# Kernel optimization log

Measured on AMD Instinct MI355X. Metric: run time of the kernel, lower is better.

The kernel has to match this reference:

```python
import jax, jax.numpy as jnp
import numpy as np

B, T, IN, H = 64, 256, 512, 1024


def setup_inputs() -> dict:
    key = jax.random.key(0)
    ks = jax.random.split(key, 21)
    stdv = 1.0 / float(np.sqrt(H))
    u = lambda k, shape: jax.random.uniform(k, shape, jnp.float32, -stdv, stdv)
    inp = {"input": jax.random.normal(ks[0], (B, T, IN), jnp.float32)}
    idx = 1
    for g in ("f", "i", "o", "c"):
        inp[f"W_{g}"] = u(ks[idx], (H, IN)); idx += 1
        inp[f"W_{g}_mask"] = u(ks[idx], (H, IN)); idx += 1
        inp[f"U_{g}"] = u(ks[idx], (H, H)); idx += 1
        inp[f"U_{g}_mask"] = u(ks[idx], (H, H)); idx += 1
        inp[f"b_{g}"] = u(ks[idx], (H,)); idx += 1
    return inp


def reference(input, W_f, W_f_mask, U_f, U_f_mask, b_f,
              W_i, W_i_mask, U_i, U_i_mask, b_i,
              W_o, W_o_mask, U_o, U_o_mask, b_o,
              W_c, W_c_mask, U_c, U_c_mask, b_c):
    # MaskedParameterMatrix with wise='feat': sigmoid(x @ W_mask^T) * (x @ W^T)
    def ml(x, W, Wm):
        return jax.nn.sigmoid(x @ Wm.T) * (x @ W.T)

    def step(carry, x_t):  # x_t: [B, IN]
        h, c = carry  # each [B, H]
        f = jax.nn.sigmoid(ml(x_t, W_f, W_f_mask) + ml(h, U_f, U_f_mask) + b_f)
        # NOTE: original module computes the input gate but never uses it (bug kept for fidelity)
        i = jax.nn.sigmoid(ml(x_t, W_i, W_i_mask) + ml(h, U_i, U_i_mask) + b_i)
        o = jax.nn.sigmoid(ml(x_t, W_o, W_o_mask) + ml(h, U_o, U_o_mask) + b_o)
        c = f * c + jnp.tanh(ml(x_t, W_c, W_c_mask) + ml(h, U_c, U_c_mask) + b_c)
        h = o * c
        return (h, c), h

    b, hdim = input.shape[0], W_f.shape[0]
    h0 = jnp.zeros((b, hdim), input.dtype)
    (hT, cT), ys = jax.lax.scan(step, (h0, h0), jnp.swapaxes(input, 0, 1))
    output = jnp.swapaxes(ys, 0, 1)  # [B, T, H]
    # final states shaped [1, B, H] as in the torch module (after transpose)
    return output, (hT[None], cT[None])
```

## Files before the change

kernel.cpp:

```cpp
#include <hip/hip_runtime.h>
#include <hip/hip_bf16.h>


typedef __attribute__((ext_vector_type(8))) short bfrag;
typedef __attribute__((ext_vector_type(4))) float f32x4;

__device__ __forceinline__ unsigned short f2b(float v) {
  __hip_bfloat16 h = __float2bfloat16(v);
  union { __hip_bfloat16 h; unsigned short u; } c; c.h = h; return c.u;
}
__device__ __forceinline__ float b2f(unsigned short u) {
  union { unsigned int i; float f; } c; c.i = ((unsigned int)u) << 16; return c.f;
}
__device__ __forceinline__ float sigm(float x) { return 1.0f / (1.0f + __expf(-x)); }
__device__ __forceinline__ float tanh_f(float x) {
  float e = __expf(2.0f * x);
  return (e - 1.0f) / (e + 1.0f);
}

__global__ __launch_bounds__(512, 2) void xproj_kernel(
    const float* __restrict__ inp,
    const float* __restrict__ Wf, const float* __restrict__ Wmf,
    const float* __restrict__ Wo, const float* __restrict__ Wmo,
    const float* __restrict__ Wc, const float* __restrict__ Wmc,
    unsigned short* __restrict__ mlx)
{
  __shared__ unsigned short Al[256 * 128];
  __shared__ unsigned short Bl[256 * 128];

  const int tid = threadIdx.x;
  const int w = tid >> 6, l = tid & 63;
  const int c = l & 15, g4 = l >> 4;
  const int jc = blockIdx.x, gate = blockIdx.y, tq = blockIdx.z;
  const float* W  = (gate == 0) ? Wf  : (gate == 1) ? Wo  : Wc;
  const float* Wm = (gate == 0) ? Wmf : (gate == 1) ? Wmo : Wmc;
  const int j0 = jc * 128;

  f32x4 acc[2][16];
#pragma unroll
  for (int mi = 0; mi < 2; ++mi)
#pragma unroll
    for (int ni = 0; ni < 16; ++ni) acc[mi][ni] = (f32x4){0.f, 0.f, 0.f, 0.f};

  for (int kc = 0; kc < 4; ++kc) {
#pragma unroll
    for (int i = 0; i < 16; ++i) {
      int idx = tid + i * 512;
      int row = idx >> 5;
      int xl  = idx & 31;
      int b_ = row & 63, tl = row >> 6;
      const float4 va = *(const float4*)(inp + (size_t)(b_ * 256 + tq * 4 + tl) * 512 + kc * 128 + xl * 4);
      ushort4 pa;
      pa.x = f2b(va.x); pa.y = f2b(va.y); pa.z = f2b(va.z); pa.w = f2b(va.w);
      *(ushort4*)((char*)Al + ((row * 256 + xl * 8) ^ ((row & 7) << 4))) = pa;
      const float* src = (row < 128) ? (W + (size_t)(j0 + row) * 512)
                                     : (Wm + (size_t)(j0 + row - 128) * 512);
      const float4 vb = *(const float4*)(src + kc * 128 + xl * 4);
      ushort4 pb;
      pb.x = f2b(vb.x); pb.y = f2b(vb.y); pb.z = f2b(vb.z); pb.w = f2b(vb.w);
      *(ushort4*)((char*)Bl + ((row * 256 + xl * 8) ^ ((row & 7) << 4))) = pb;
    }
    __syncthreads();
#pragma unroll
    for (int ks = 0; ks < 4; ++ks) {
      const int koff = (ks * 32 + g4 * 8) * 2;
      bfrag af[2];
#pragma unroll
      for (int mi = 0; mi < 2; ++mi) {
        int row = w * 32 + mi * 16 + c;
        af[mi] = *(const bfrag*)((const char*)Al + ((row * 256 + koff) ^ ((row & 7) << 4)));
      }
#pragma unroll
      for (int ni = 0; ni < 16; ++ni) {
        int n = ni * 16 + c;
        bfrag bf = *(const bfrag*)((const char*)Bl + ((n * 256 + koff) ^ ((n & 7) << 4)));
#pragma unroll
        for (int mi = 0; mi < 2; ++mi)
          acc[mi][ni] = __builtin_amdgcn_mfma_f32_16x16x32_bf16(af[mi], bf, acc[mi][ni], 0, 0, 0);
      }
    }
    __syncthreads();
  }
#pragma unroll
  for (int mi = 0; mi < 2; ++mi) {
#pragma unroll
    for (int ni = 0; ni < 8; ++ni) {
      f32x4 xw = acc[mi][ni];
      f32x4 xm = acc[mi][ni + 8];
      ushort4 st;
      st.x = f2b(xw[0] * sigm(xm[0]));
      st.y = f2b(xw[1] * sigm(xm[1]));
      st.z = f2b(xw[2] * sigm(xm[2]));
      st.w = f2b(xw[3] * sigm(xm[3]));
      int row = w * 32 + mi * 16 + g4 * 4;
      int tl = row >> 6, b_ = row & 63;
      int j = j0 + ni * 16 + c;
      size_t addr = ((size_t)((tq * 4 + tl) * 3 + gate) * 1024 + j) * 64 + b_;
      *(ushort4*)(mlx + addr) = st;
    }
  }
}

__global__ __launch_bounds__(256, 1) void recur_kernel(
    const float* __restrict__ Uf, const float* __restrict__ Umf,
    const float* __restrict__ Uo, const float* __restrict__ Umo,
    const float* __restrict__ Uc, const float* __restrict__ Umc,
    const float* __restrict__ bfp, const float* __restrict__ bop,
    const float* __restrict__ bcp,
    const unsigned short* __restrict__ mlx,
    unsigned short* __restrict__ hx,
    float* __restrict__ cfin,
    unsigned int* __restrict__ sent)
{
  __shared__ float prep[2][4 * 48 * 68];

  __builtin_amdgcn_fence(__ATOMIC_ACQUIRE, "agent");

  const int tid = threadIdx.x;
  const int bid = blockIdx.x;
  const int w = tid >> 6, l = tid & 63;
  const int c = l & 15, g4 = l >> 4;
  const int j0 = bid * 8;

  bfrag Breg[3][8];
#pragma unroll
  for (int nt = 0; nt < 3; ++nt) {
    const int n = nt * 16 + c;
    const int mi6 = n >> 3;
    const float* src = (mi6 == 0) ? Uf : (mi6 == 1) ? Umf : (mi6 == 2) ? Uo
                     : (mi6 == 3) ? Umo : (mi6 == 4) ? Uc : Umc;
    src += (size_t)(j0 + (n & 7)) * 1024;
#pragma unroll
    for (int ks = 0; ks < 8; ++ks) {
      const int k = w * 256 + ks * 32 + g4 * 8;
      const float4 v0 = *(const float4*)(src + k);
      const float4 v1 = *(const float4*)(src + k + 4);
      bfrag b;
      b[0] = (short)f2b(v0.x); b[1] = (short)f2b(v0.y);
      b[2] = (short)f2b(v0.z); b[3] = (short)f2b(v0.w);
      b[4] = (short)f2b(v1.x); b[5] = (short)f2b(v1.y);
      b[6] = (short)f2b(v1.z); b[7] = (short)f2b(v1.w);
      Breg[nt][ks] = b;
    }
  }

  const int bb = l;
  const int cl0 = w * 2;
  float bias[2][3], cr[2] = {0.f, 0.f};
  float mf[2], mo[2], mc[2];
#pragma unroll
  for (int q = 0; q < 2; ++q) {
    bias[q][0] = bfp[j0 + cl0 + q];
    bias[q][1] = bop[j0 + cl0 + q];
    bias[q][2] = bcp[j0 + cl0 + q];
  }
  {
    size_t mb = (size_t)(j0 + cl0) * 64 + bb;
#pragma unroll
    for (int q = 0; q < 2; ++q) {
      mf[q] = b2f(mlx[mb + q * 64]);
      mo[q] = b2f(mlx[mb + 65536 + q * 64]);
      mc[q] = b2f(mlx[mb + 2 * 65536 + q * 64]);
    }
  }

  for (int t = 0; t < 256; ++t) {
    if (t > 0) {
      const unsigned long long* sp =
          (const unsigned long long*)(sent + (size_t)t * 512 + w * 128 + 2 * l);
      while (true) {
        unsigned long long v = __hip_atomic_load(sp, __ATOMIC_RELAXED, __HIP_MEMORY_SCOPE_AGENT);
        if (__all(v == 0x0000000100000001ULL)) break;
      }
      __builtin_amdgcn_sched_barrier(0);
      asm volatile("" ::: "memory");
    }

    f32x4 acc[4][3];
#pragma unroll
    for (int mi = 0; mi < 4; ++mi)
#pragma unroll
      for (int nt = 0; nt < 3; ++nt) acc[mi][nt] = (f32x4){0.f, 0.f, 0.f, 0.f};

#pragma unroll
    for (int ks = 0; ks < 8; ++ks) {
      const int kb = w * 32 + ks * 4 + g4;
#pragma unroll
      for (int mi = 0; mi < 4; ++mi) {
        const bfrag af = *(const bfrag*)(hx + (((size_t)t * 128 + kb) * 64 + mi * 16 + c) * 8);
#pragma unroll
        for (int nt = 0; nt < 3; ++nt)
          acc[mi][nt] = __builtin_amdgcn_mfma_f32_16x16x32_bf16(af, Breg[nt][ks], acc[mi][nt], 0, 0, 0);
      }
    }
    float* pp = prep[t & 1];
#pragma unroll
    for (int mi = 0; mi < 4; ++mi)
#pragma unroll
      for (int nt = 0; nt < 3; ++nt) {
        int col = nt * 16 + c;
        *(f32x4*)&pp[(w * 48 + col) * 68 + mi * 16 + g4 * 4] = acc[mi][nt];
      }
    __syncthreads();

    unsigned int pack = 0;
#pragma unroll
    for (int q = 0; q < 2; ++q) {
      const int cl = cl0 + q;
      float s[6];
#pragma unroll
      for (int m = 0; m < 6; ++m) {
        const int col = m * 8 + cl;
        s[m] = pp[col * 68 + bb] + pp[(48 + col) * 68 + bb] +
               pp[(96 + col) * 68 + bb] + pp[(144 + col) * 68 + bb];
      }
      float fg = sigm(mf[q] + sigm(s[1]) * s[0] + bias[q][0]);
      float og = sigm(mo[q] + sigm(s[3]) * s[2] + bias[q][1]);
      float cd = tanh_f(mc[q] + sigm(s[5]) * s[4] + bias[q][2]);
      cr[q] = fg * cr[q] + cd;
      float hv = og * cr[q];
      pack |= (unsigned int)f2b(hv) << (16 * q);
      if (t == 255) cfin[(size_t)(j0 + cl) * 64 + bb] = cr[q];
    }
    __hip_atomic_store(
        (unsigned int*)(hx + ((((size_t)(t + 1) * 128 + bid) * 64 + bb) * 8 + cl0)),
        pack, __ATOMIC_RELAXED, __HIP_MEMORY_SCOPE_AGENT);

    asm volatile("s_waitcnt vmcnt(0)" ::: "memory");
    if (l == 0)
      __hip_atomic_store(&sent[(size_t)(t + 1) * 512 + bid * 4 + w], 1u,
                         __ATOMIC_RELAXED, __HIP_MEMORY_SCOPE_AGENT);

    if (t < 255) {
      size_t mb = (size_t)(t + 1) * 3 * 65536 + (size_t)(j0 + cl0) * 64 + bb;
#pragma unroll
      for (int q = 0; q < 2; ++q) {
        mf[q] = b2f(mlx[mb + q * 64]);
        mo[q] = b2f(mlx[mb + 65536 + q * 64]);
        mc[q] = b2f(mlx[mb + 2 * 65536 + q * 64]);
      }
    }
  }
}

__global__ __launch_bounds__(128) void histcast_kernel(
    const unsigned short* __restrict__ hx, float* __restrict__ out)
{
  const int b = blockIdx.x >> 8, t = blockIdx.x & 255;
  const int j = threadIdx.x * 8;
  const unsigned short* src = hx + (((size_t)(t + 1) * 128 + (j >> 3)) * 64 + b) * 8;
  float* dst = out + ((size_t)b * 256 + t) * 1024 + j;
  ushort4 v0 = *(const ushort4*)(src);
  ushort4 v1 = *(const ushort4*)(src + 4);
  float4 o0, o1;
  o0.x = b2f(v0.x); o0.y = b2f(v0.y); o0.z = b2f(v0.z); o0.w = b2f(v0.w);
  o1.x = b2f(v1.x); o1.y = b2f(v1.y); o1.z = b2f(v1.z); o1.w = b2f(v1.w);
  *(float4*)(dst) = o0;
  *(float4*)(dst + 4) = o1;
}

__global__ __launch_bounds__(256) void finals_kernel(
    const unsigned short* __restrict__ hx, const float* __restrict__ cfin,
    float* __restrict__ out)
{
  int tid = blockIdx.x * 256 + threadIdx.x;
  int b = tid >> 10, j = tid & 1023;
  out[16777216 + tid]         = b2f(hx[(((size_t)256 * 128 + (j >> 3)) * 64 + b) * 8 + (j & 7)]);
  out[16777216 + 65536 + tid] = cfin[(size_t)j * 64 + b];
}

extern "C" void kernel_launch(void* const* d_in, const int* in_sizes, int n_in,
                              void* d_out, int out_size, void* d_ws, size_t ws_size,
                              hipStream_t stream)
{
  const float* input = (const float*)d_in[0];
  const float* W_f  = (const float*)d_in[1];
  const float* Wm_f = (const float*)d_in[2];
  const float* U_f  = (const float*)d_in[3];
  const float* Um_f = (const float*)d_in[4];
  const float* b_f  = (const float*)d_in[5];
  const float* W_o  = (const float*)d_in[11];
  const float* Wm_o = (const float*)d_in[12];
  const float* U_o  = (const float*)d_in[13];
  const float* Um_o = (const float*)d_in[14];
  const float* b_o  = (const float*)d_in[15];
  const float* W_c  = (const float*)d_in[16];
  const float* Wm_c = (const float*)d_in[17];
  const float* U_c  = (const float*)d_in[18];
  const float* Um_c = (const float*)d_in[19];
  const float* b_c  = (const float*)d_in[20];

  char* ws = (char*)d_ws;
  size_t off = 0;
  unsigned short* mlx = (unsigned short*)(ws + off); off += (size_t)256 * 3 * 1024 * 64 * 2;
  unsigned short* hx  = (unsigned short*)(ws + off); off += (size_t)257 * 128 * 64 * 8 * 2;
  float* cfin = (float*)(ws + off);                  off += (size_t)1024 * 64 * 4;
  unsigned int* sent = (unsigned int*)(ws + off);    off += (size_t)257 * 512 * 4;
  if (off > ws_size) return;

  hipMemsetAsync(hx, 0, 131072, stream);
  hipMemsetAsync(sent, 0, (size_t)257 * 512 * 4, stream);

  xproj_kernel<<<dim3(8, 3, 64), 512, 0, stream>>>(input, W_f, Wm_f, W_o, Wm_o, W_c, Wm_c, mlx);
  recur_kernel<<<128, 256, 0, stream>>>(U_f, Um_f, U_o, Um_o, U_c, Um_c,
                                        b_f, b_o, b_c, mlx, hx, cfin, sent);
  histcast_kernel<<<16384, 128, 0, stream>>>(hx, (float*)d_out);
  finals_kernel<<<256, 256, 0, stream>>>(hx, cfin, (float*)d_out);
}
```

Baseline: 2.271 ms.

## Replace sentinel-flag handshake with data-as-flag polling on hidden state

Removes the separate per-step sentinel array. The hidden-state buffer is now pre-filled with 0xFF and consumers spin directly on the h values until no 32-bit word is all-ones, so the data itself acts as the ready signal. This drops the vmcnt wait and flag store on the producer side and one round trip of latency per step. The mask-projection loads are moved to the top of each step. The cost is a large extra memset of the history buffer and a correctness assumption that two adjacent bf16 values never both encode 0xFFFF (a NaN pattern).

```diff
diff --git a/kernel.cpp b/kernel.cpp
--- a/kernel.cpp
+++ b/kernel.cpp
@@ -109,8 +109,7 @@
     const float* __restrict__ bcp,
     const unsigned short* __restrict__ mlx,
     unsigned short* __restrict__ hx,
-    float* __restrict__ cfin,
-    unsigned int* __restrict__ sent)
+    float* __restrict__ cfin)
 {
   __shared__ float prep[2][4 * 48 * 68];
 
@@ -147,33 +146,23 @@
   const int bb = l;
   const int cl0 = w * 2;
   float bias[2][3], cr[2] = {0.f, 0.f};
-  float mf[2], mo[2], mc[2];
 #pragma unroll
   for (int q = 0; q < 2; ++q) {
     bias[q][0] = bfp[j0 + cl0 + q];
     bias[q][1] = bop[j0 + cl0 + q];
     bias[q][2] = bcp[j0 + cl0 + q];
   }
-  {
-    size_t mb = (size_t)(j0 + cl0) * 64 + bb;
-#pragma unroll
-    for (int q = 0; q < 2; ++q) {
-      mf[q] = b2f(mlx[mb + q * 64]);
-      mo[q] = b2f(mlx[mb + 65536 + q * 64]);
-      mc[q] = b2f(mlx[mb + 2 * 65536 + q * 64]);
-    }
-  }
 
   for (int t = 0; t < 256; ++t) {
-    if (t > 0) {
-      const unsigned long long* sp =
-          (const unsigned long long*)(sent + (size_t)t * 512 + w * 128 + 2 * l);
-      while (true) {
-        unsigned long long v = __hip_atomic_load(sp, __ATOMIC_RELAXED, __HIP_MEMORY_SCOPE_AGENT);
-        if (__all(v == 0x0000000100000001ULL)) break;
-      }
-      __builtin_amdgcn_sched_barrier(0);
-      asm volatile("" ::: "memory");
+    float mfv[2], mov[2], mcv[2];
+    {
+      size_t mb = (size_t)t * 3 * 65536 + (size_t)(j0 + cl0) * 64 + bb;
+#pragma unroll
+      for (int q = 0; q < 2; ++q) {
+        mfv[q] = b2f(mlx[mb + q * 64]);
+        mov[q] = b2f(mlx[mb + 65536 + q * 64]);
+        mcv[q] = b2f(mlx[mb + 2 * 65536 + q * 64]);
+      }
     }
 
     f32x4 acc[4][3];
@@ -185,14 +174,35 @@
 #pragma unroll
     for (int ks = 0; ks < 8; ++ks) {
       const int kb = w * 32 + ks * 4 + g4;
+      const unsigned long long* rowp =
+          (const unsigned long long*)(hx + (((size_t)t * 128 + kb) * 64 + c) * 8);
+      unsigned long long q0[4], q1[4];
+      while (true) {
+        bool ok = true;
+#pragma unroll
+        for (int mi = 0; mi < 4; ++mi) {
+          q0[mi] = __hip_atomic_load(rowp + mi * 32,     __ATOMIC_RELAXED, __HIP_MEMORY_SCOPE_AGENT);
+          q1[mi] = __hip_atomic_load(rowp + mi * 32 + 1, __ATOMIC_RELAXED, __HIP_MEMORY_SCOPE_AGENT);
+        }
+#pragma unroll
+        for (int mi = 0; mi < 4; ++mi) {
+          ok = ok && ((unsigned)(q0[mi])       != 0xFFFFFFFFu)
+                  && ((unsigned)(q0[mi] >> 32) != 0xFFFFFFFFu)
+                  && ((unsigned)(q1[mi])       != 0xFFFFFFFFu)
+                  && ((unsigned)(q1[mi] >> 32) != 0xFFFFFFFFu);
+        }
+        if (__all(ok)) break;
+      }
 #pragma unroll
       for (int mi = 0; mi < 4; ++mi) {
-        const bfrag af = *(const bfrag*)(hx + (((size_t)t * 128 + kb) * 64 + mi * 16 + c) * 8);
+        union { unsigned long long q[2]; bfrag f; } u;
+        u.q[0] = q0[mi]; u.q[1] = q1[mi];
 #pragma unroll
         for (int nt = 0; nt < 3; ++nt)
-          acc[mi][nt] = __builtin_amdgcn_mfma_f32_16x16x32_bf16(af, Breg[nt][ks], acc[mi][nt], 0, 0, 0);
-      }
-    }
+          acc[mi][nt] = __builtin_amdgcn_mfma_f32_16x16x32_bf16(u.f, Breg[nt][ks], acc[mi][nt], 0, 0, 0);
+      }
+    }
+
     float* pp = prep[t & 1];
 #pragma unroll
     for (int mi = 0; mi < 4; ++mi)
@@ -214,9 +224,9 @@
         s[m] = pp[col * 68 + bb] + pp[(48 + col) * 68 + bb] +
                pp[(96 + col) * 68 + bb] + pp[(144 + col) * 68 + bb];
       }
-      float fg = sigm(mf[q] + sigm(s[1]) * s[0] + bias[q][0]);
-      float og = sigm(mo[q] + sigm(s[3]) * s[2] + bias[q][1]);
-      float cd = tanh_f(mc[q] + sigm(s[5]) * s[4] + bias[q][2]);
+      float fg = sigm(mfv[q] + sigm(s[1]) * s[0] + bias[q][0]);
+      float og = sigm(mov[q] + sigm(s[3]) * s[2] + bias[q][1]);
+      float cd = tanh_f(mcv[q] + sigm(s[5]) * s[4] + bias[q][2]);
       cr[q] = fg * cr[q] + cd;
       float hv = og * cr[q];
       pack |= (unsigned int)f2b(hv) << (16 * q);
@@ -225,21 +235,6 @@
     __hip_atomic_store(
         (unsigned int*)(hx + ((((size_t)(t + 1) * 128 + bid) * 64 + bb) * 8 + cl0)),
         pack, __ATOMIC_RELAXED, __HIP_MEMORY_SCOPE_AGENT);
-
-    asm volatile("s_waitcnt vmcnt(0)" ::: "memory");
-    if (l == 0)
-      __hip_atomic_store(&sent[(size_t)(t + 1) * 512 + bid * 4 + w], 1u,
-                         __ATOMIC_RELAXED, __HIP_MEMORY_SCOPE_AGENT);
-
-    if (t < 255) {
-      size_t mb = (size_t)(t + 1) * 3 * 65536 + (size_t)(j0 + cl0) * 64 + bb;
-#pragma unroll
-      for (int q = 0; q < 2; ++q) {
-        mf[q] = b2f(mlx[mb + q * 64]);
-        mo[q] = b2f(mlx[mb + 65536 + q * 64]);
-        mc[q] = b2f(mlx[mb + 2 * 65536 + q * 64]);
-      }
-    }
   }
 }
 
@@ -295,15 +290,14 @@
   unsigned short* mlx = (unsigned short*)(ws + off); off += (size_t)256 * 3 * 1024 * 64 * 2;
   unsigned short* hx  = (unsigned short*)(ws + off); off += (size_t)257 * 128 * 64 * 8 * 2;
   float* cfin = (float*)(ws + off);                  off += (size_t)1024 * 64 * 4;
-  unsigned int* sent = (unsigned int*)(ws + off);    off += (size_t)257 * 512 * 4;
   if (off > ws_size) return;
 
   hipMemsetAsync(hx, 0, 131072, stream);
-  hipMemsetAsync(sent, 0, (size_t)257 * 512 * 4, stream);
+  hipMemsetAsync((char*)hx + 131072, 0xFF, (size_t)256 * 131072, stream);
 
   xproj_kernel<<<dim3(8, 3, 64), 512, 0, stream>>>(input, W_f, Wm_f, W_o, Wm_o, W_c, Wm_c, mlx);
   recur_kernel<<<128, 256, 0, stream>>>(U_f, Um_f, U_o, Um_o, U_c, Um_c,
-                                        b_f, b_o, b_c, mlx, hx, cfin, sent);
+                                        b_f, b_o, b_c, mlx, hx, cfin);
   histcast_kernel<<<16384, 128, 0, stream>>>(hx, (float*)d_out);
   finals_kernel<<<256, 256, 0, stream>>>(hx, cfin, (float*)d_out);
 }
```

After: 2.405 ms. 5.9% more time.

## Move recurrent weights to swizzled LDS, batch h loads, coalesce h stores via LDS

Applied to the files above, without the earlier changes.

Recurrent weight fragments now live in an XOR-swizzled LDS buffer instead of registers, and are read per k-step during the MFMA loop. All h fragments for a step are loaded up front before any MFMA. Each wave's packed h outputs are gathered in LDS and written as 64-bit atomic stores by 16 lanes instead of 32-bit stores from every lane. The double-buffered prep array becomes single-buffered, and the per-step mlx loads move before the spin-wait. The aim is to free registers and raise memory-level parallelism, at the cost of extra LDS traffic and an added __syncthreads per step on the serial critical path.

```diff
diff --git a/kernel.cpp b/kernel.cpp
--- a/kernel.cpp
+++ b/kernel.cpp
@@ -112,7 +112,9 @@
     float* __restrict__ cfin,
     unsigned int* __restrict__ sent)
 {
-  __shared__ float prep[2][4 * 48 * 68];
+  __shared__ unsigned short Blds[48 * 1024];
+  __shared__ float prep[4 * 48 * 68];
+  __shared__ unsigned int hshare[64 * 4];
 
   __builtin_amdgcn_fence(__ATOMIC_ACQUIRE, "agent");
 
@@ -122,49 +124,49 @@
   const int c = l & 15, g4 = l >> 4;
   const int j0 = bid * 8;
 
-  bfrag Breg[3][8];
-#pragma unroll
-  for (int nt = 0; nt < 3; ++nt) {
-    const int n = nt * 16 + c;
-    const int mi6 = n >> 3;
-    const float* src = (mi6 == 0) ? Uf : (mi6 == 1) ? Umf : (mi6 == 2) ? Uo
-                     : (mi6 == 3) ? Umo : (mi6 == 4) ? Uc : Umc;
-    src += (size_t)(j0 + (n & 7)) * 1024;
-#pragma unroll
-    for (int ks = 0; ks < 8; ++ks) {
-      const int k = w * 256 + ks * 32 + g4 * 8;
-      const float4 v0 = *(const float4*)(src + k);
-      const float4 v1 = *(const float4*)(src + k + 4);
-      bfrag b;
-      b[0] = (short)f2b(v0.x); b[1] = (short)f2b(v0.y);
-      b[2] = (short)f2b(v0.z); b[3] = (short)f2b(v0.w);
-      b[4] = (short)f2b(v1.x); b[5] = (short)f2b(v1.y);
-      b[6] = (short)f2b(v1.z); b[7] = (short)f2b(v1.w);
-      Breg[nt][ks] = b;
+  {
+    const float* mats[6] = {Uf, Umf, Uo, Umo, Uc, Umc};
+    const int rbase = tid >> 4;
+    const int sub = tid & 15;
+#pragma unroll
+    for (int rep = 0; rep < 3; ++rep) {
+      int r = rep * 16 + rbase;
+      const float* src = mats[r >> 3] + (size_t)(j0 + (r & 7)) * 1024;
+#pragma unroll
+      for (int i = 0; i < 16; ++i) {
+        int k = sub * 64 + i * 4;
+        float4 v = *(const float4*)(src + k);
+        ushort4 p;
+        p.x = f2b(v.x); p.y = f2b(v.y); p.z = f2b(v.z); p.w = f2b(v.w);
+        *(ushort4*)((char*)Blds + (((r * 1024 + k) * 2) ^ ((r & 7) << 4))) = p;
+      }
     }
   }
 
   const int bb = l;
   const int cl0 = w * 2;
   float bias[2][3], cr[2] = {0.f, 0.f};
-  float mf[2], mo[2], mc[2];
 #pragma unroll
   for (int q = 0; q < 2; ++q) {
     bias[q][0] = bfp[j0 + cl0 + q];
     bias[q][1] = bop[j0 + cl0 + q];
     bias[q][2] = bcp[j0 + cl0 + q];
   }
-  {
-    size_t mb = (size_t)(j0 + cl0) * 64 + bb;
-#pragma unroll
-    for (int q = 0; q < 2; ++q) {
-      mf[q] = b2f(mlx[mb + q * 64]);
-      mo[q] = b2f(mlx[mb + 65536 + q * 64]);
-      mc[q] = b2f(mlx[mb + 2 * 65536 + q * 64]);
-    }
-  }
+  const int kb0 = (w * 256 + g4 * 8) * 2;
+  __syncthreads();
 
   for (int t = 0; t < 256; ++t) {
+    float mfv[2], mov[2], mcv[2];
+    {
+      size_t mb = (size_t)t * 3 * 65536 + (size_t)(j0 + cl0) * 64 + bb;
+#pragma unroll
+      for (int q = 0; q < 2; ++q) {
+        mfv[q] = b2f(mlx[mb + q * 64]);
+        mov[q] = b2f(mlx[mb + 65536 + q * 64]);
+        mcv[q] = b2f(mlx[mb + 2 * 65536 + q * 64]);
+      }
+    }
+
     if (t > 0) {
       const unsigned long long* sp =
           (const unsigned long long*)(sent + (size_t)t * 512 + w * 128 + 2 * l);
@@ -176,30 +178,44 @@
       asm volatile("" ::: "memory");
     }
 
-    f32x4 acc[4][3];
-#pragma unroll
-    for (int mi = 0; mi < 4; ++mi)
-#pragma unroll
-      for (int nt = 0; nt < 3; ++nt) acc[mi][nt] = (f32x4){0.f, 0.f, 0.f, 0.f};
-
+    bfrag af[8][4];
 #pragma unroll
     for (int ks = 0; ks < 8; ++ks) {
       const int kb = w * 32 + ks * 4 + g4;
-#pragma unroll
-      for (int mi = 0; mi < 4; ++mi) {
-        const bfrag af = *(const bfrag*)(hx + (((size_t)t * 128 + kb) * 64 + mi * 16 + c) * 8);
+      const unsigned short* rp = hx + (((size_t)t * 128 + kb) * 64 + c) * 8;
+#pragma unroll
+      for (int mi = 0; mi < 4; ++mi)
+        af[ks][mi] = *(const bfrag*)(rp + mi * 16 * 8);
+    }
+
+    f32x4 acc[4][3];
+#pragma unroll
+    for (int mi = 0; mi < 4; ++mi)
+#pragma unroll
+      for (int nt = 0; nt < 3; ++nt) acc[mi][nt] = (f32x4){0.f, 0.f, 0.f, 0.f};
+
+#pragma unroll
+    for (int ks = 0; ks < 8; ++ks) {
+      const int kb2 = kb0 + ks * 64;
+      bfrag bfr[3];
+#pragma unroll
+      for (int nt = 0; nt < 3; ++nt) {
+        const int n = nt * 16 + c;
+        bfr[nt] = *(const bfrag*)((const char*)Blds + (n * 2048 + (kb2 ^ ((n & 7) << 4))));
+      }
+#pragma unroll
+      for (int mi = 0; mi < 4; ++mi)
 #pragma unroll
         for (int nt = 0; nt < 3; ++nt)
-          acc[mi][nt] = __builtin_amdgcn_mfma_f32_16x16x32_bf16(af, Breg[nt][ks], acc[mi][nt], 0, 0, 0);
-      }
-    }
-    float* pp = prep[t & 1];
+          acc[mi][nt] = __builtin_amdgcn_mfma_f32_16x16x32_bf16(af[ks][mi], bfr[nt], acc[mi][nt], 0, 0, 0);
+    }
+
 #pragma unroll
     for (int mi = 0; mi < 4; ++mi)
 #pragma unroll
       for (int nt = 0; nt < 3; ++nt) {
         int col = nt * 16 + c;
-        *(f32x4*)&pp[(w * 48 + col) * 68 + mi * 16 + g4 * 4] = acc[mi][nt];
+        *(f32x4*)&prep[(w * 48 + col) * 68 + mi * 16 + g4 * 4] = acc[mi][nt];
       }
     __syncthreads();
 
@@ -211,35 +227,35 @@
 #pragma unroll
       for (int m = 0; m < 6; ++m) {
         const int col = m * 8 + cl;
-        s[m] = pp[col * 68 + bb] + pp[(48 + col) * 68 + bb] +
-               pp[(96 + col) * 68 + bb] + pp[(144 + col) * 68 + bb];
-      }
-      float fg = sigm(mf[q] + sigm(s[1]) * s[0] + bias[q][0]);
-      float og = sigm(mo[q] + sigm(s[3]) * s[2] + bias[q][1]);
-      float cd = tanh_f(mc[q] + sigm(s[5]) * s[4] + bias[q][2]);
+        s[m] = prep[col * 68 + bb] + prep[(48 + col) * 68 + bb] +
+               prep[(96 + col) * 68 + bb] + prep[(144 + col) * 68 + bb];
+      }
+      float fg = sigm(mfv[q] + sigm(s[1]) * s[0] + bias[q][0]);
+      float og = sigm(mov[q] + sigm(s[3]) * s[2] + bias[q][1]);
+      float cd = tanh_f(mcv[q] + sigm(s[5]) * s[4] + bias[q][2]);
       cr[q] = fg * cr[q] + cd;
       float hv = og * cr[q];
       pack |= (unsigned int)f2b(hv) << (16 * q);
       if (t == 255) cfin[(size_t)(j0 + cl) * 64 + bb] = cr[q];
     }
-    __hip_atomic_store(
-        (unsigned int*)(hx + ((((size_t)(t + 1) * 128 + bid) * 64 + bb) * 8 + cl0)),
-        pack, __ATOMIC_RELAXED, __HIP_MEMORY_SCOPE_AGENT);
-
+
+    hshare[bb * 4 + w] = pack;
+    __syncthreads();
+
+    if (l < 16) {
+      const int row = w * 16 + l;
+      const uint4 hv4 = *(const uint4*)&hshare[row * 4];
+      unsigned long long q0 = ((unsigned long long)hv4.y << 32) | hv4.x;
+      unsigned long long q1 = ((unsigned long long)hv4.w << 32) | hv4.z;
+      unsigned long long* dst =
+          (unsigned long long*)(hx + ((((size_t)(t + 1) * 128 + bid) * 64 + row) * 8));
+      __hip_atomic_store(dst,     q0, __ATOMIC_RELAXED, __HIP_MEMORY_SCOPE_AGENT);
+      __hip_atomic_store(dst + 1, q1, __ATOMIC_RELAXED, __HIP_MEMORY_SCOPE_AGENT);
+    }
     asm volatile("s_waitcnt vmcnt(0)" ::: "memory");
     if (l == 0)
       __hip_atomic_store(&sent[(size_t)(t + 1) * 512 + bid * 4 + w], 1u,
                          __ATOMIC_RELAXED, __HIP_MEMORY_SCOPE_AGENT);
-
-    if (t < 255) {
-      size_t mb = (size_t)(t + 1) * 3 * 65536 + (size_t)(j0 + cl0) * 64 + bb;
-#pragma unroll
-      for (int q = 0; q < 2; ++q) {
-        mf[q] = b2f(mlx[mb + q * 64]);
-        mo[q] = b2f(mlx[mb + 65536 + q * 64]);
-        mc[q] = b2f(mlx[mb + 2 * 65536 + q * 64]);
-      }
-    }
   }
 }
 
```

Result: slower. 2.640 ms (+16.2%).

## Split batch into four 16-row groups and pipeline recurrence across them per wave

Applied to the files above, without the earlier changes.

The recurrent kernel now gives each wave two hidden columns over the full K dimension, with all 32 K-chunks of U held in registers. The batch is split into four independent 16-row groups that are processed in a staggered software pipeline. While one group's MFMA runs, the previous group's gate math, h store and flag signalling proceed, and the next group's flags are polled. This removes the cross-wave LDS reduction and the block-wide __syncthreads, and hides the inter-block flag latency behind independent work. In exchange it uses many more registers, finer-grained flags (four times as many sync points) and a changed hx layout.

```diff
diff --git a/kernel.cpp b/kernel.cpp
--- a/kernel.cpp
+++ b/kernel.cpp
@@ -112,7 +112,7 @@
     float* __restrict__ cfin,
     unsigned int* __restrict__ sent)
 {
-  __shared__ float prep[2][4 * 48 * 68];
+  __shared__ float ldsT[4][16][17];
 
   __builtin_amdgcn_fence(__ATOMIC_ACQUIRE, "agent");
 
@@ -120,127 +120,138 @@
   const int bid = blockIdx.x;
   const int w = tid >> 6, l = tid & 63;
   const int c = l & 15, g4 = l >> 4;
-  const int j0 = bid * 8;
-
-  bfrag Breg[3][8];
-#pragma unroll
-  for (int nt = 0; nt < 3; ++nt) {
-    const int n = nt * 16 + c;
-    const int mi6 = n >> 3;
-    const float* src = (mi6 == 0) ? Uf : (mi6 == 1) ? Umf : (mi6 == 2) ? Uo
-                     : (mi6 == 3) ? Umo : (mi6 == 4) ? Uc : Umc;
-    src += (size_t)(j0 + (n & 7)) * 1024;
-#pragma unroll
-    for (int ks = 0; ks < 8; ++ks) {
-      const int k = w * 256 + ks * 32 + g4 * 8;
-      const float4 v0 = *(const float4*)(src + k);
-      const float4 v1 = *(const float4*)(src + k + 4);
-      bfrag b;
-      b[0] = (short)f2b(v0.x); b[1] = (short)f2b(v0.y);
-      b[2] = (short)f2b(v0.z); b[3] = (short)f2b(v0.w);
-      b[4] = (short)f2b(v1.x); b[5] = (short)f2b(v1.y);
-      b[6] = (short)f2b(v1.z); b[7] = (short)f2b(v1.w);
-      Breg[nt][ks] = b;
+  const int W = bid * 4 + w;
+  const int r = c;
+  const int q = g4 & 1;
+
+  bfrag Breg[32];
+  {
+    const int m = c >> 1, q2 = c & 1;
+    const float* up = (m == 0) ? Uf : (m == 1) ? Umf : (m == 2) ? Uo
+                    : (m == 3) ? Umo : (m == 4) ? Uc : Umc;
+    const float* src = up + (size_t)(2 * W + q2) * 1024;
+    const bool pad = (c >= 12);
+#pragma unroll
+    for (int kc = 0; kc < 32; ++kc) {
+      bfrag b = {0, 0, 0, 0, 0, 0, 0, 0};
+      if (!pad) {
+        const float4 v0 = *(const float4*)(src + kc * 32 + g4 * 8);
+        const float4 v1 = *(const float4*)(src + kc * 32 + g4 * 8 + 4);
+        b[0] = (short)f2b(v0.x); b[1] = (short)f2b(v0.y);
+        b[2] = (short)f2b(v0.z); b[3] = (short)f2b(v0.w);
+        b[4] = (short)f2b(v1.x); b[5] = (short)f2b(v1.y);
+        b[6] = (short)f2b(v1.z); b[7] = (short)f2b(v1.w);
+      }
+      Breg[kc] = b;
     }
   }
-
-  const int bb = l;
-  const int cl0 = w * 2;
-  float bias[2][3], cr[2] = {0.f, 0.f};
-  float mf[2], mo[2], mc[2];
-#pragma unroll
-  for (int q = 0; q < 2; ++q) {
-    bias[q][0] = bfp[j0 + cl0 + q];
-    bias[q][1] = bop[j0 + cl0 + q];
-    bias[q][2] = bcp[j0 + cl0 + q];
+  const float bf_ = bfp[2 * W + q], bo_ = bop[2 * W + q], bc_ = bcp[2 * W + q];
+
+  bfrag af[32];
+  f32x4 accA = {0.f,0.f,0.f,0.f}, accB = {0.f,0.f,0.f,0.f};
+  float crA = 0.f, crB = 0.f, crC = 0.f, crD = 0.f;
+  unsigned long long P0[4] = {0,0,0,0}, P1[4] = {0,0,0,0};
+  float mA0=0.f,mA1=0.f,mA2=0.f, mB0=0.f,mB1=0.f,mB2=0.f;
+  const unsigned long long SOK = 0x0000000100000001ULL;
+
+#define SLOT(Pp, ACCP, ACCC, CR, MI0, MI1, MI2, MO0, MO1, MO2, PCHK, PNEW)     \
+  do {                                                                         \
+    const int s_ = t4 * 4 + (Pp);                                              \
+              \
+    if (t4 > 0) {                                                              \
+      f32x4 c0={0.f,0.f,0.f,0.f}, c1={0.f,0.f,0.f,0.f};                        \
+      f32x4 c2={0.f,0.f,0.f,0.f}, c3={0.f,0.f,0.f,0.f};                        \
+      _Pragma("unroll")                                                        \
+      for (int kc = 0; kc < 32; kc += 4) {                                     \
+        c0 = __builtin_amdgcn_mfma_f32_16x16x32_bf16(af[kc+0], Breg[kc+0], c0, 0,0,0); \
+        c1 = __builtin_amdgcn_mfma_f32_16x16x32_bf16(af[kc+1], Breg[kc+1], c1, 0,0,0); \
+        c2 = __builtin_amdgcn_mfma_f32_16x16x32_bf16(af[kc+2], Breg[kc+2], c2, 0,0,0); \
+        c3 = __builtin_amdgcn_mfma_f32_16x16x32_bf16(af[kc+3], Breg[kc+3], c3, 0,0,0); \
+      }                                                                        \
+      ACCC = (c0 + c1) + (c2 + c3);                                            \
+    } else {                                                                   \
+      ACCC = (f32x4){0.f, 0.f, 0.f, 0.f};                                      \
+    }                                                                          \
+         \
+    asm volatile("s_waitcnt vmcnt(0)" ::: "memory");                           \
+    if (s_ >= 2 && l == 0)                                                     \
+      __hip_atomic_store(&sent[(size_t)(s_ + 2) * 512 + W], 1u,                \
+                         __ATOMIC_RELAXED, __HIP_MEMORY_SCOPE_AGENT);          \
+         \
+    if ((s_ + 1) >= 4 && (s_ + 1) <= 1023) {                                   \
+      while (true) {                                                           \
+        bool ok = (PCHK[0] == SOK) && (PCHK[1] == SOK) &&                      \
+                  (PCHK[2] == SOK) && (PCHK[3] == SOK);                        \
+        if (__all(ok)) break;                                                  \
+        const unsigned long long* pp =                                         \
+            (const unsigned long long*)(sent + (size_t)(s_ + 1) * 512) + 4*l;  \
+        PCHK[0] = __hip_atomic_load(pp+0, __ATOMIC_RELAXED, __HIP_MEMORY_SCOPE_AGENT); \
+        PCHK[1] = __hip_atomic_load(pp+1, __ATOMIC_RELAXED, __HIP_MEMORY_SCOPE_AGENT); \
+        PCHK[2] = __hip_atomic_load(pp+2, __ATOMIC_RELAXED, __HIP_MEMORY_SCOPE_AGENT); \
+        PCHK[3] = __hip_atomic_load(pp+3, __ATOMIC_RELAXED, __HIP_MEMORY_SCOPE_AGENT); \
+      }                                                                        \
+      __builtin_amdgcn_sched_barrier(0);                                       \
+      asm volatile("" ::: "memory");                                           \
+      const unsigned short* ap = hx + (size_t)(s_ + 1) * 16384 + c * 1024 + g4 * 8; \
+      _Pragma("unroll")                                                        \
+      for (int kc = 0; kc < 32; ++kc) af[kc] = *(const bfrag*)(ap + kc * 32);  \
+    }                                                                          \
+            \
+    if (s_ >= 1) {                                                             \
+      const int tl = ((Pp) >= 1) ? t4 : (t4 - 1);                              \
+      const int gl = ((Pp) + 3) & 3;                                           \
+      ldsT[w][g4 * 4 + 0][c] = ACCP[0];                                        \
+      ldsT[w][g4 * 4 + 1][c] = ACCP[1];                                        \
+      ldsT[w][g4 * 4 + 2][c] = ACCP[2];                                        \
+      ldsT[w][g4 * 4 + 3][c] = ACCP[3];                                        \
+      float s0 = ldsT[w][r][0 + q], s1 = ldsT[w][r][2 + q];                    \
+      float s2 = ldsT[w][r][4 + q], s3 = ldsT[w][r][6 + q];                    \
+      float s4 = ldsT[w][r][8 + q], s5 = ldsT[w][r][10 + q];                   \
+      float fg = sigm((MI0) + sigm(s1) * s0 + bf_);                            \
+      float og = sigm((MI1) + sigm(s3) * s2 + bo_);                            \
+      float cd = tanh_f((MI2) + sigm(s5) * s4 + bc_);                          \
+      CR = fg * CR + cd;                                                       \
+      float hv = og * CR;                                                      \
+      unsigned int hvu = f2b(hv);                                              \
+      unsigned int hi = (unsigned int)__shfl((int)hvu, (l + 16) & 63, 64);     \
+      unsigned int pack = (hvu & 0xFFFFu) | (hi << 16);                        \
+      if (l < 16)                                                              \
+        __hip_atomic_store(                                                    \
+            (unsigned int*)(hx + (size_t)(s_ + 3) * 16384 + l * 1024 + 2 * W), \
+            pack, __ATOMIC_RELAXED, __HIP_MEMORY_SCOPE_AGENT);                 \
+      if (tl == 255 && l < 32)                                                 \
+        cfin[(size_t)(2 * W + q) * 64 + gl * 16 + r] = CR;                     \
+    }                                                                          \
+                                            \
+    if ((s_ + 2) >= 4 && (s_ + 2) <= 1023) {                                   \
+      const unsigned long long* pp =                                           \
+          (const unsigned long long*)(sent + (size_t)(s_ + 2) * 512) + 4 * l;  \
+      PNEW[0] = __hip_atomic_load(pp+0, __ATOMIC_RELAXED, __HIP_MEMORY_SCOPE_AGENT); \
+      PNEW[1] = __hip_atomic_load(pp+1, __ATOMIC_RELAXED, __HIP_MEMORY_SCOPE_AGENT); \
+      PNEW[2] = __hip_atomic_load(pp+2, __ATOMIC_RELAXED, __HIP_MEMORY_SCOPE_AGENT); \
+      PNEW[3] = __hip_atomic_load(pp+3, __ATOMIC_RELAXED, __HIP_MEMORY_SCOPE_AGENT); \
+    }                                                                          \
+                \
+    if (s_ <= 1023) {                                                          \
+      size_t mb = ((size_t)t4 * 3 * 1024 + (2 * W + q)) * 64 + (Pp) * 16 + r;  \
+      MO0 = b2f(mlx[mb]);                                                      \
+      MO1 = b2f(mlx[mb + 65536]);                                              \
+      MO2 = b2f(mlx[mb + 131072]);                                             \
+    }                                                                          \
+  } while (0)
+
+#pragma unroll 1
+  for (int t4 = 0; t4 < 256; ++t4) {
+    SLOT(0, accB, accA, crD, mB0, mB1, mB2, mA0, mA1, mA2, P1, P0);
+    SLOT(1, accA, accB, crA, mA0, mA1, mA2, mB0, mB1, mB2, P0, P1);
+    SLOT(2, accB, accA, crB, mB0, mB1, mB2, mA0, mA1, mA2, P1, P0);
+    SLOT(3, accA, accB, crC, mA0, mA1, mA2, mB0, mB1, mB2, P0, P1);
   }
   {
-    size_t mb = (size_t)(j0 + cl0) * 64 + bb;
-#pragma unroll
-    for (int q = 0; q < 2; ++q) {
-      mf[q] = b2f(mlx[mb + q * 64]);
-      mo[q] = b2f(mlx[mb + 65536 + q * 64]);
-      mc[q] = b2f(mlx[mb + 2 * 65536 + q * 64]);
-    }
-  }
-
-  for (int t = 0; t < 256; ++t) {
-    if (t > 0) {
-      const unsigned long long* sp =
-          (const unsigned long long*)(sent + (size_t)t * 512 + w * 128 + 2 * l);
-      while (true) {
-        unsigned long long v = __hip_atomic_load(sp, __ATOMIC_RELAXED, __HIP_MEMORY_SCOPE_AGENT);
-        if (__all(v == 0x0000000100000001ULL)) break;
-      }
-      __builtin_amdgcn_sched_barrier(0);
-      asm volatile("" ::: "memory");
-    }
-
-    f32x4 acc[4][3];
-#pragma unroll
-    for (int mi = 0; mi < 4; ++mi)
-#pragma unroll
-      for (int nt = 0; nt < 3; ++nt) acc[mi][nt] = (f32x4){0.f, 0.f, 0.f, 0.f};
-
-#pragma unroll
-    for (int ks = 0; ks < 8; ++ks) {
-      const int kb = w * 32 + ks * 4 + g4;
-#pragma unroll
-      for (int mi = 0; mi < 4; ++mi) {
-        const bfrag af = *(const bfrag*)(hx + (((size_t)t * 128 + kb) * 64 + mi * 16 + c) * 8);
-#pragma unroll
-        for (int nt = 0; nt < 3; ++nt)
-          acc[mi][nt] = __builtin_amdgcn_mfma_f32_16x16x32_bf16(af, Breg[nt][ks], acc[mi][nt], 0, 0, 0);
-      }
-    }
-    float* pp = prep[t & 1];
-#pragma unroll
-    for (int mi = 0; mi < 4; ++mi)
-#pragma unroll
-      for (int nt = 0; nt < 3; ++nt) {
-        int col = nt * 16 + c;
-        *(f32x4*)&pp[(w * 48 + col) * 68 + mi * 16 + g4 * 4] = acc[mi][nt];
-      }
-    __syncthreads();
-
-    unsigned int pack = 0;
-#pragma unroll
-    for (int q = 0; q < 2; ++q) {
-      const int cl = cl0 + q;
-      float s[6];
-#pragma unroll
-      for (int m = 0; m < 6; ++m) {
-        const int col = m * 8 + cl;
-        s[m] = pp[col * 68 + bb] + pp[(48 + col) * 68 + bb] +
-               pp[(96 + col) * 68 + bb] + pp[(144 + col) * 68 + bb];
-      }
-      float fg = sigm(mf[q] + sigm(s[1]) * s[0] + bias[q][0]);
-      float og = sigm(mo[q] + sigm(s[3]) * s[2] + bias[q][1]);
-      float cd = tanh_f(mc[q] + sigm(s[5]) * s[4] + bias[q][2]);
-      cr[q] = fg * cr[q] + cd;
-      float hv = og * cr[q];
-      pack |= (unsigned int)f2b(hv) << (16 * q);
-      if (t == 255) cfin[(size_t)(j0 + cl) * 64 + bb] = cr[q];
-    }
-    __hip_atomic_store(
-        (unsigned int*)(hx + ((((size_t)(t + 1) * 128 + bid) * 64 + bb) * 8 + cl0)),
-        pack, __ATOMIC_RELAXED, __HIP_MEMORY_SCOPE_AGENT);
-
-    asm volatile("s_waitcnt vmcnt(0)" ::: "memory");
-    if (l == 0)
-      __hip_atomic_store(&sent[(size_t)(t + 1) * 512 + bid * 4 + w], 1u,
-                         __ATOMIC_RELAXED, __HIP_MEMORY_SCOPE_AGENT);
-
-    if (t < 255) {
-      size_t mb = (size_t)(t + 1) * 3 * 65536 + (size_t)(j0 + cl0) * 64 + bb;
-#pragma unroll
-      for (int q = 0; q < 2; ++q) {
-        mf[q] = b2f(mlx[mb + q * 64]);
-        mo[q] = b2f(mlx[mb + 65536 + q * 64]);
-        mc[q] = b2f(mlx[mb + 2 * 65536 + q * 64]);
-      }
-    }
-  }
+    const int t4 = 256;
+    SLOT(0, accB, accA, crD, mB0, mB1, mB2, mA0, mA1, mA2, P1, P0);
+  }
+#undef SLOT
 }
 
 __global__ __launch_bounds__(128) void histcast_kernel(
@@ -248,7 +259,8 @@
 {
   const int b = blockIdx.x >> 8, t = blockIdx.x & 255;
   const int j = threadIdx.x * 8;
-  const unsigned short* src = hx + (((size_t)(t + 1) * 128 + (j >> 3)) * 64 + b) * 8;
+  const unsigned short* src =
+      hx + (size_t)((t + 1) * 4 + (b >> 4)) * 16384 + (b & 15) * 1024 + j;
   float* dst = out + ((size_t)b * 256 + t) * 1024 + j;
   ushort4 v0 = *(const ushort4*)(src);
   ushort4 v1 = *(const ushort4*)(src + 4);
@@ -265,7 +277,8 @@
 {
   int tid = blockIdx.x * 256 + threadIdx.x;
   int b = tid >> 10, j = tid & 1023;
-  out[16777216 + tid]         = b2f(hx[(((size_t)256 * 128 + (j >> 3)) * 64 + b) * 8 + (j & 7)]);
+  out[16777216 + tid] =
+      b2f(hx[(size_t)(1024 + (b >> 4)) * 16384 + (b & 15) * 1024 + j]);
   out[16777216 + 65536 + tid] = cfin[(size_t)j * 64 + b];
 }
 
@@ -293,13 +306,12 @@
   char* ws = (char*)d_ws;
   size_t off = 0;
   unsigned short* mlx = (unsigned short*)(ws + off); off += (size_t)256 * 3 * 1024 * 64 * 2;
-  unsigned short* hx  = (unsigned short*)(ws + off); off += (size_t)257 * 128 * 64 * 8 * 2;
+  unsigned short* hx  = (unsigned short*)(ws + off); off += (size_t)1028 * 16384 * 2;
   float* cfin = (float*)(ws + off);                  off += (size_t)1024 * 64 * 4;
-  unsigned int* sent = (unsigned int*)(ws + off);    off += (size_t)257 * 512 * 4;
+  unsigned int* sent = (unsigned int*)(ws + off);    off += (size_t)1028 * 512 * 4;
   if (off > ws_size) return;
 
-  hipMemsetAsync(hx, 0, 131072, stream);
-  hipMemsetAsync(sent, 0, (size_t)257 * 512 * 4, stream);
+  hipMemsetAsync(sent, 0, (size_t)1028 * 512 * 4, stream);
 
   xproj_kernel<<<dim3(8, 3, 64), 512, 0, stream>>>(input, W_f, Wm_f, W_o, Wm_o, W_c, Wm_c, mlx);
   recur_kernel<<<128, 256, 0, stream>>>(U_f, Um_f, U_o, Um_o, U_c, Um_c,
```

New measurement: 5.249 ms. +131.1%, slower.
